# Kernel optimization log

Measured on AMD Instinct MI355X. Metric: run time of the kernel, lower is better.

The kernel has to match this reference:

```python
import jax, jax.numpy as jnp
import numpy as np

GAMMA = 0.99          # discount factor from __init__
TD_LAMBDA = 0.95      # lambda for GAE (lambda < 1 -> GAE branch)
STEP_TYPE_LAST = 2    # alf StepType.LAST


def setup_inputs() -> dict:
    key = jax.random.key(0)
    k0, k1, k2, k3, k4 = jax.random.split(key, 5)
    T1, B = 1024, 4096  # [T+1, B] time-major
    return {
        "value": jax.random.normal(k0, (T1, B), jnp.float32),
        "target_value": jax.random.normal(k1, (T1, B), jnp.float32),
        "reward": jax.random.normal(k2, (T1, B), jnp.float32),
        "step_type": jax.random.randint(k3, (T1, B), 0, 3, jnp.int32),
        "discount": jax.random.uniform(k4, (T1, B), dtype=jnp.float32),
    }


def _gae(reward, target_value, step_type, discount):
    # discounts passed to value_ops are training_info.discount * gamma
    d = discount * GAMMA                                   # [T+1, B]
    is_last = (step_type == STEP_TYPE_LAST).astype(reward.dtype)
    # one-step TD residuals, time-major [T, B]
    delta = reward[1:] + d[1:] * target_value[1:] - target_value[:-1]
    wd = d[1:] * TD_LAMBDA                                 # [T, B]
    not_last = 1.0 - is_last[:-1]                          # [T, B]

    def step(adv_next, xs):
        delta_t, wd_t, nl_t = xs
        adv = nl_t * (delta_t + wd_t * adv_next)
        return adv, adv

    init = jnp.zeros_like(reward[0])                       # [B]
    _, advs = jax.lax.scan(step, init, (delta, wd, not_last), reverse=True)
    return advs                                            # [T, B]


def reference(value, target_value, reward, step_type, discount):
    advs = jax.lax.stop_gradient(_gae(reward, target_value, step_type, discount))
    returns = advs + target_value[:-1]                     # G_t^lambda, [T, B]
    # element_wise_squared_loss(returns.detach(), value[:-1])
    td_err = jax.lax.stop_gradient(returns) - value[:-1]
    loss = td_err * td_err                                 # [T, B]
    # tensor_extend_zero: append a zero row -> [T+1, B]
    return jnp.concatenate([loss, jnp.zeros_like(loss[:1])], axis=0)
```

## Files before the change

### kernel.cpp

```cpp
#include <hip/hip_runtime.h>

#define T1     1024
#define T      1023
#define B      4096
#define Q      1024
#define CHUNK  16
#define NCHUNK 64
#define GPC    4

#define GAMMA     0.99f
#define TD_LAMBDA 0.95f

typedef __attribute__((ext_vector_type(4))) float f4;
typedef __attribute__((ext_vector_type(4))) int   i4;

__global__ __launch_bounds__(256) void k_compose(
    const float* __restrict__ tv, const float* __restrict__ rew,
    const int* __restrict__ st, const float* __restrict__ disc,
    float* __restrict__ AggA, float* __restrict__ AggB)
{
    int c = blockIdx.x >> 2;
    int g = blockIdx.x & 3;
    int q = (g << 8) + threadIdx.x;
    int s = c * CHUNK;
    int e = min(s + CHUNK, T);

    const f4* tv4   = (const f4*)tv;
    const f4* rew4  = (const f4*)rew;
    const f4* disc4 = (const f4*)disc;
    const i4* st4   = (const i4*)st;

    f4 A  = {0.f, 0.f, 0.f, 0.f};
    f4 Bf = {1.f, 1.f, 1.f, 1.f};
    f4 tvn = tv4[(size_t)e * Q + q];
#pragma unroll 4
    for (int t = e - 1; t >= s; --t) {
        size_t i  = (size_t)t * Q + q;
        size_t i1 = i + Q;
        f4 d1  = disc4[i1] * GAMMA;
        f4 tvt = tv4[i];
        f4 r1  = rew4[i1];
        i4 stt = st4[i];
#pragma unroll
        for (int j = 0; j < 4; ++j) {
            float delta = r1[j] + d1[j] * tvn[j] - tvt[j];
            float wd    = d1[j] * TD_LAMBDA;
            float nl    = (stt[j] == 2) ? 0.f : 1.f;
            float a  = nl * delta;
            float bb = nl * wd;
            A[j]  = fmaf(bb, A[j], a);
            Bf[j] *= bb;
        }
        tvn = tvt;
    }
    ((f4*)AggA)[c * Q + q] = A;
    ((f4*)AggB)[c * Q + q] = Bf;
}

__global__ __launch_bounds__(256) void k_replay(
    const float* __restrict__ value, const float* __restrict__ tv,
    const float* __restrict__ rew, const int* __restrict__ st,
    const float* __restrict__ disc,
    const float* __restrict__ AggA, const float* __restrict__ AggB,
    float* __restrict__ out)
{
    int c = blockIdx.x >> 2;
    int g = blockIdx.x & 3;
    int q = (g << 8) + threadIdx.x;
    int s = c * CHUNK;
    int e = min(s + CHUNK, T);

    const f4* tv4   = (const f4*)tv;
    const f4* rew4  = (const f4*)rew;
    const f4* disc4 = (const f4*)disc;
    const f4* val4  = (const f4*)value;
    const i4* st4   = (const i4*)st;
    const f4* A4    = (const f4*)AggA;
    const f4* B4    = (const f4*)AggB;
    f4* out4 = (f4*)out;

    f4 S = {0.f, 0.f, 0.f, 0.f};
    f4 P = {1.f, 1.f, 1.f, 1.f};
    for (int cc = c + 1; cc < NCHUNK; ++cc) {
        f4 a = A4[cc * Q + q];
        f4 b = B4[cc * Q + q];
#pragma unroll
        for (int j = 0; j < 4; ++j) {
            S[j] = fmaf(P[j], a[j], S[j]);
            P[j] *= b[j];
        }
    }
    f4 adv = S;

    if (c == NCHUNK - 1) {
        f4 z = {0.f, 0.f, 0.f, 0.f};
        out4[(size_t)T * Q + q] = z;
    }

    f4 tvn = tv4[(size_t)e * Q + q];
#pragma unroll 4
    for (int t = e - 1; t >= s; --t) {
        size_t i  = (size_t)t * Q + q;
        size_t i1 = i + Q;
        f4 d1  = disc4[i1] * GAMMA;
        f4 tvt = tv4[i];
        f4 r1  = rew4[i1];
        i4 stt = st4[i];
        f4 vv  = val4[i];
        f4 o;
#pragma unroll
        for (int j = 0; j < 4; ++j) {
            float delta = r1[j] + d1[j] * tvn[j] - tvt[j];
            float wd    = d1[j] * TD_LAMBDA;
            float nl    = (stt[j] == 2) ? 0.f : 1.f;
            adv[j] = nl * fmaf(wd, adv[j], delta);
            float td = adv[j] + tvt[j] - vv[j];
            o[j] = td * td;
        }
        out4[i] = o;
        tvn = tvt;
    }
}

extern "C" void kernel_launch(void* const* d_in, const int* in_sizes, int n_in,
                              void* d_out, int out_size, void* d_ws, size_t ws_size,
                              hipStream_t stream) {
    const float* value = (const float*)d_in[0];
    const float* tv    = (const float*)d_in[1];
    const float* rew   = (const float*)d_in[2];
    const int*   st    = (const int*)d_in[3];
    const float* disc  = (const float*)d_in[4];
    float* out = (float*)d_out;

    float* AggA = (float*)d_ws;
    float* AggB = AggA + (size_t)NCHUNK * B;

    k_compose<<<NCHUNK * GPC, 256, 0, stream>>>(tv, rew, st, disc, AggA, AggB);
    k_replay<<<NCHUNK * GPC, 256, 0, stream>>>(value, tv, rew, st, disc, AggA, AggB, out);
}
```

Measured before the change: 133.7 us.

## Fuse compose and replay into one cooperative kernel with LDS-retained per-step terms

Merges the two chunked-scan kernels into a single cooperative launch separated by a grid-wide sync. During the compose pass each thread keeps the per-step scan coefficients and tv-minus-value for the first 12 timesteps of its chunk in LDS, so the replay pass rereads global inputs only for the remaining 4 steps. This removes one kernel launch and most of the second read of the five input arrays. In exchange it adds a grid barrier, uses about 144 KB of shared memory per block, and depends on all 256 blocks being co-resident.

Result: slower. 177.3 us (+32.6%).

```diff
diff --git a/kernel.cpp b/kernel.cpp
--- a/kernel.cpp
+++ b/kernel.cpp
@@ -1,4 +1,7 @@
 #include <hip/hip_runtime.h>
+#include <hip/hip_cooperative_groups.h>
+
+namespace cg = cooperative_groups;
 
 #define T1     1024
 #define T      1023
@@ -7,6 +10,8 @@
 #define CHUNK  16
 #define NCHUNK 64
 #define GPC    4
+#define QB     256
+#define RETAIN 12
 
 #define GAMMA     0.99f
 #define TD_LAMBDA 0.95f
@@ -14,11 +19,17 @@
 typedef __attribute__((ext_vector_type(4))) float f4;
 typedef __attribute__((ext_vector_type(4))) int   i4;
 
-__global__ __launch_bounds__(256) void k_compose(
-    const float* __restrict__ tv, const float* __restrict__ rew,
-    const int* __restrict__ st, const float* __restrict__ disc,
-    float* __restrict__ AggA, float* __restrict__ AggB)
+__global__ __launch_bounds__(256) void k_fused(
+    const float* __restrict__ value, const float* __restrict__ tv,
+    const float* __restrict__ rew, const int* __restrict__ st,
+    const float* __restrict__ disc,
+    float* __restrict__ AggA, float* __restrict__ AggB,
+    float* __restrict__ out)
 {
+    __shared__ f4 a_lds[RETAIN][QB];
+    __shared__ f4 b_lds[RETAIN][QB];
+    __shared__ f4 m_lds[RETAIN][QB];
+
     int c = blockIdx.x >> 2;
     int g = blockIdx.x & 3;
     int q = (g << 8) + threadIdx.x;
@@ -28,7 +39,11 @@
     const f4* tv4   = (const f4*)tv;
     const f4* rew4  = (const f4*)rew;
     const f4* disc4 = (const f4*)disc;
+    const f4* val4  = (const f4*)value;
     const i4* st4   = (const i4*)st;
+    f4* A4 = (f4*)AggA;
+    f4* B4 = (f4*)AggB;
+    f4* out4 = (f4*)out;
 
     f4 A  = {0.f, 0.f, 0.f, 0.f};
     f4 Bf = {1.f, 1.f, 1.f, 1.f};
@@ -41,53 +56,40 @@
         f4 tvt = tv4[i];
         f4 r1  = rew4[i1];
         i4 stt = st4[i];
+        f4 a, bb;
 #pragma unroll
         for (int j = 0; j < 4; ++j) {
             float delta = r1[j] + d1[j] * tvn[j] - tvt[j];
             float wd    = d1[j] * TD_LAMBDA;
             float nl    = (stt[j] == 2) ? 0.f : 1.f;
-            float a  = nl * delta;
-            float bb = nl * wd;
-            A[j]  = fmaf(bb, A[j], a);
-            Bf[j] *= bb;
+            a[j]  = nl * delta;
+            bb[j] = nl * wd;
+            A[j]  = fmaf(bb[j], A[j], a[j]);
+            Bf[j] *= bb[j];
+        }
+        int r = t - s;
+        if (r < RETAIN) {
+            f4 vv = val4[i];
+            a_lds[r][threadIdx.x] = a;
+            b_lds[r][threadIdx.x] = bb;
+            m_lds[r][threadIdx.x] = tvt - vv;
         }
         tvn = tvt;
     }
-    ((f4*)AggA)[c * Q + q] = A;
-    ((f4*)AggB)[c * Q + q] = Bf;
-}
+    A4[c * Q + q] = A;
+    B4[c * Q + q] = Bf;
 
-__global__ __launch_bounds__(256) void k_replay(
-    const float* __restrict__ value, const float* __restrict__ tv,
-    const float* __restrict__ rew, const int* __restrict__ st,
-    const float* __restrict__ disc,
-    const float* __restrict__ AggA, const float* __restrict__ AggB,
-    float* __restrict__ out)
-{
-    int c = blockIdx.x >> 2;
-    int g = blockIdx.x & 3;
-    int q = (g << 8) + threadIdx.x;
-    int s = c * CHUNK;
-    int e = min(s + CHUNK, T);
-
-    const f4* tv4   = (const f4*)tv;
-    const f4* rew4  = (const f4*)rew;
-    const f4* disc4 = (const f4*)disc;
-    const f4* val4  = (const f4*)value;
-    const i4* st4   = (const i4*)st;
-    const f4* A4    = (const f4*)AggA;
-    const f4* B4    = (const f4*)AggB;
-    f4* out4 = (f4*)out;
+    cg::this_grid().sync();
 
     f4 S = {0.f, 0.f, 0.f, 0.f};
     f4 P = {1.f, 1.f, 1.f, 1.f};
     for (int cc = c + 1; cc < NCHUNK; ++cc) {
-        f4 a = A4[cc * Q + q];
-        f4 b = B4[cc * Q + q];
+        f4 aa = A4[cc * Q + q];
+        f4 bb = B4[cc * Q + q];
 #pragma unroll
         for (int j = 0; j < 4; ++j) {
-            S[j] = fmaf(P[j], a[j], S[j]);
-            P[j] *= b[j];
+            S[j] = fmaf(P[j], aa[j], S[j]);
+            P[j] *= bb[j];
         }
     }
     f4 adv = S;
@@ -97,9 +99,9 @@
         out4[(size_t)T * Q + q] = z;
     }
 
-    f4 tvn = tv4[(size_t)e * Q + q];
-#pragma unroll 4
-    for (int t = e - 1; t >= s; --t) {
+    f4 tvn2 = tv4[(size_t)e * Q + q];
+#pragma unroll
+    for (int t = e - 1; t >= s + RETAIN; --t) {
         size_t i  = (size_t)t * Q + q;
         size_t i1 = i + Q;
         f4 d1  = disc4[i1] * GAMMA;
@@ -110,7 +112,7 @@
         f4 o;
 #pragma unroll
         for (int j = 0; j < 4; ++j) {
-            float delta = r1[j] + d1[j] * tvn[j] - tvt[j];
+            float delta = r1[j] + d1[j] * tvn2[j] - tvt[j];
             float wd    = d1[j] * TD_LAMBDA;
             float nl    = (stt[j] == 2) ? 0.f : 1.f;
             adv[j] = nl * fmaf(wd, adv[j], delta);
@@ -118,7 +120,23 @@
             o[j] = td * td;
         }
         out4[i] = o;
-        tvn = tvt;
+        tvn2 = tvt;
+    }
+
+#pragma unroll
+    for (int r = RETAIN - 1; r >= 0; --r) {
+        size_t i = (size_t)(s + r) * Q + q;
+        f4 aa = a_lds[r][threadIdx.x];
+        f4 bb = b_lds[r][threadIdx.x];
+        f4 mm = m_lds[r][threadIdx.x];
+        f4 o;
+#pragma unroll
+        for (int j = 0; j < 4; ++j) {
+            adv[j] = fmaf(bb[j], adv[j], aa[j]);
+            float td = adv[j] + mm[j];
+            o[j] = td * td;
+        }
+        out4[i] = o;
     }
 }
 
@@ -135,6 +153,8 @@
     float* AggA = (float*)d_ws;
     float* AggB = AggA + (size_t)NCHUNK * B;
 
-    k_compose<<<NCHUNK * GPC, 256, 0, stream>>>(tv, rew, st, disc, AggA, AggB);
-    k_replay<<<NCHUNK * GPC, 256, 0, stream>>>(value, tv, rew, st, disc, AggA, AggB, out);
+    void* args[] = {(void*)&value, (void*)&tv, (void*)&rew, (void*)&st,
+                    (void*)&disc, (void*)&AggA, (void*)&AggB, (void*)&out};
+    hipLaunchCooperativeKernel((void*)k_fused, dim3(NCHUNK * GPC), dim3(256),
+                               args, 0, stream);
 }
```
